# Optimization experiments

Hardware: AMD Instinct MI355X
Metric: run time of the kernel (lower is better)

## Reference

```python
import jax, jax.numpy as jnp
import numpy as np

N = 100000   # nodes
E = 1600000  # edges
IN_DIM = 256
HID = 128
OUT_DIM = 64
LAYERS = 3
LN_EPS = 1e-5


def _layer_norm(y, g, b):
    mu = jnp.mean(y, axis=-1, keepdims=True)
    var = jnp.mean(jnp.square(y - mu), axis=-1, keepdims=True)
    return (y - mu) * jax.lax.rsqrt(var + LN_EPS) * g + b


def _gcn_conv(x, W, b, src, dst, norm):
    # x: [N, H]; W: [H, H]; src/dst: [E+N] (self-loops appended); norm: [E+N]
    xw = x @ W
    msg = xw[src] * norm[:, None]                       # [E+N, H] gather
    out = jax.ops.segment_sum(msg, dst, num_segments=N)  # scatter-add
    return out + b


def setup_inputs() -> dict:
    key = jax.random.key(0)
    ks = jax.random.split(key, 8)
    x = jax.random.normal(ks[0], (N, IN_DIM), dtype=jnp.float32)
    edge_index = jax.random.randint(ks[1], (2, E), 0, N, dtype=jnp.int32)
    in_W = jax.random.normal(ks[2], (IN_DIM, HID), dtype=jnp.float32) / np.sqrt(IN_DIM).astype(np.float32)
    in_b = jnp.zeros((HID,), jnp.float32)
    conv_W = jax.random.normal(ks[3], (LAYERS, HID, HID), dtype=jnp.float32) / np.sqrt(HID).astype(np.float32)
    conv_b = jnp.zeros((LAYERS, HID), jnp.float32)
    ln_g = jnp.ones((LAYERS, HID), jnp.float32)
    ln_b = jnp.zeros((LAYERS, HID), jnp.float32)
    out_W = jax.random.normal(ks[4], (HID, OUT_DIM), dtype=jnp.float32) / np.sqrt(HID).astype(np.float32)
    out_b = jnp.zeros((OUT_DIM,), jnp.float32)
    return {"x": x, "edge_index": edge_index, "in_W": in_W, "in_b": in_b,
            "conv_W": conv_W, "conv_b": conv_b, "ln_g": ln_g, "ln_b": ln_b,
            "out_W": out_W, "out_b": out_b}


def reference(x, edge_index, in_W, in_b, conv_W, conv_b, ln_g, ln_b, out_W, out_b):
    # add self loops (GCNConv add_self_loops=True, edge_weight=None -> ones)
    loops = jnp.arange(N, dtype=edge_index.dtype)
    src = jnp.concatenate([edge_index[0], loops])
    dst = jnp.concatenate([edge_index[1], loops])
    # symmetric normalization: deg over destination, norm = d^-1/2[src]*d^-1/2[dst]
    deg = jax.ops.segment_sum(jnp.ones_like(src, dtype=jnp.float32), dst, num_segments=N)
    dinv = jnp.where(deg > 0, jax.lax.rsqrt(deg), 0.0)
    norm = dinv[src] * dinv[dst]

    h = x @ in_W + in_b
    for i in range(LAYERS):
        y = _gcn_conv(h, conv_W[i], conv_b[i], src, dst, norm)
        y = _layer_norm(y, ln_g[i], ln_b[i])
        y = jax.nn.relu(y)
        h = h + y  # residual (dropout is identity in eval mode)
    return h @ out_W + out_b
```

## Files before the change

### kernel.cpp

```cpp
#include <hip/hip_runtime.h>
#include <hip/hip_bf16.h>

#define N_NODES 100000
#define E_EDGES 1600000
#define IN_DIM  256
#define HID     128
#define OUT_DIM 64
#define LAYERS  3
#define LN_EPS  1e-5f

typedef __attribute__((ext_vector_type(8)))  short bf16x8;
typedef __attribute__((ext_vector_type(16))) float f32x16;

__device__ inline short f2bf(float f) {
    unsigned u = __float_as_uint(f);
    unsigned r = (u + 0x7fffu + ((u >> 16) & 1u)) >> 16;
    return (short)r;
}
__device__ inline float bflo(unsigned u) { return __uint_as_float(u << 16); }
__device__ inline float bfhi(unsigned u) { return __uint_as_float(u & 0xffff0000u); }


__global__ __launch_bounds__(256) void deg_kernel(const int* __restrict__ dst, int* __restrict__ deg) {
    int e = blockIdx.x * 256 + threadIdx.x;
    if (e < E_EDGES) atomicAdd(&deg[dst[e]], 1);
}

__global__ __launch_bounds__(256) void dinv_kernel(const int* __restrict__ deg, float* __restrict__ dinv) {
    int i = blockIdx.x * 256 + threadIdx.x;
    if (i < N_NODES) dinv[i] = rsqrtf((float)(deg[i] + 1));
}


#define NB_SCAN ((N_NODES + 255) / 256)

__global__ __launch_bounds__(256) void block_sum_kernel(const int* __restrict__ deg,
                                                        int* __restrict__ blockSums) {
    __shared__ int s[256];
    int i = blockIdx.x * 256 + threadIdx.x;
    s[threadIdx.x] = (i < N_NODES) ? deg[i] : 0;
    __syncthreads();
#pragma unroll
    for (int o = 128; o; o >>= 1) {
        if (threadIdx.x < o) s[threadIdx.x] += s[threadIdx.x + o];
        __syncthreads();
    }
    if (threadIdx.x == 0) blockSums[blockIdx.x] = s[0];
}

__global__ __launch_bounds__(512) void scan_blocks_kernel(int* __restrict__ blockSums, int nb) {
    __shared__ int s[512];
    int t = threadIdx.x;
    int orig = (t < nb) ? blockSums[t] : 0;
    s[t] = orig;
    __syncthreads();
#pragma unroll
    for (int o = 1; o < 512; o <<= 1) {
        int v = (t >= o) ? s[t - o] : 0;
        __syncthreads();
        s[t] += v;
        __syncthreads();
    }
    if (t < nb) blockSums[t] = s[t] - orig;
}

__global__ __launch_bounds__(256) void scan_final_kernel(const int* __restrict__ deg,
                                                         const int* __restrict__ blockSums,
                                                         int* __restrict__ offsets,
                                                         int* __restrict__ cursor) {
    __shared__ int s[256];
    int i = blockIdx.x * 256 + threadIdx.x;
    int t = threadIdx.x;
    int v = (i < N_NODES) ? deg[i] : 0;
    s[t] = v;
    __syncthreads();
#pragma unroll
    for (int o = 1; o < 256; o <<= 1) {
        int u = (t >= o) ? s[t - o] : 0;
        __syncthreads();
        s[t] += u;
        __syncthreads();
    }
    if (i < N_NODES) {
        int excl = s[t] - v + blockSums[blockIdx.x];
        offsets[i] = excl;
        cursor[i] = excl;
    }
}

__global__ __launch_bounds__(256) void bin_kernel(const int* __restrict__ src,
                                                  const int* __restrict__ dst,
                                                  const float* __restrict__ dinv,
                                                  int* __restrict__ cursor,
                                                  int2* __restrict__ es) {
    int e = blockIdx.x * 256 + threadIdx.x;
    if (e >= E_EDGES) return;
    int s = src[e], d = dst[e];
    int p = atomicAdd(&cursor[d], 1);
    es[p] = make_int2(s, __float_as_int(dinv[s] * dinv[d]));
}


template<int K, int N>
__global__ __launch_bounds__(256) void wt_kernel(const float* __restrict__ W, short* __restrict__ WT) {
    int idx = blockIdx.x * 256 + threadIdx.x;
    if (idx >= K * N) return;
    int n = idx / K, k = idx % K;
    WT[idx] = f2bf(W[(long)k * N + n]);
}


template<int KT, int N, bool ABF>
__global__ __launch_bounds__(256) void mfma_gemm(const void* __restrict__ Av,
                                                 const short* __restrict__ WT,
                                                 const float* __restrict__ bias,
                                                 float* __restrict__ C,
                                                 short* __restrict__ Cb,
                                                 int M) {
    constexpr int BK = 128;
    constexpr int SR = BK * 2 + 16;
    constexpr int NT = N / 32;

    __shared__ char lds[N * SR];

    const int tid = threadIdx.x;
    const int wv = tid >> 6;
    const int ln = tid & 63;
    const int l31 = ln & 31;
    const int lh = ln >> 5;
    const int row_base = blockIdx.x * 256 + wv * 64;

    f32x16 acc[2][NT];
#pragma unroll
    for (int rt = 0; rt < 2; rt++)
#pragma unroll
        for (int nt = 0; nt < NT; nt++)
#pragma unroll
            for (int r = 0; r < 16; r++) acc[rt][nt][r] = 0.f;

    long aoff[2];
#pragma unroll
    for (int rt = 0; rt < 2; rt++) {
        int r = row_base + rt * 32 + l31;
        if (r > M - 1) r = M - 1;
        aoff[rt] = (long)r * KT + lh * 8;
    }

#pragma unroll
    for (int c = 0; c < KT / BK; c++) {
        __syncthreads();
#pragma unroll
        for (int i = tid; i < N * 16; i += 256) {
            int n = i >> 4, kb = (i & 15) << 4;
            float4 v = *(const float4*)((const char*)WT + (long)n * (KT * 2) + c * (BK * 2) + kb);
            *(float4*)(&lds[n * SR + kb]) = v;
        }
        __syncthreads();

#pragma unroll
        for (int ks = 0; ks < BK / 16; ks++) {
            bf16x8 a[2];
#pragma unroll
            for (int rt = 0; rt < 2; rt++) {
                if (ABF) {
                    a[rt] = *(const bf16x8*)((const short*)Av + aoff[rt] + c * BK + ks * 16);
                } else {
                    const float* ap = (const float*)Av + aoff[rt] + c * BK + ks * 16;
                    float4 f0 = *(const float4*)(ap);
                    float4 f1 = *(const float4*)(ap + 4);
                    bf16x8 t;
                    t[0] = f2bf(f0.x); t[1] = f2bf(f0.y); t[2] = f2bf(f0.z); t[3] = f2bf(f0.w);
                    t[4] = f2bf(f1.x); t[5] = f2bf(f1.y); t[6] = f2bf(f1.z); t[7] = f2bf(f1.w);
                    a[rt] = t;
                }
            }
            bf16x8 b[NT];
#pragma unroll
            for (int nt = 0; nt < NT; nt++) {
                int n = nt * 32 + l31;
                b[nt] = *(const bf16x8*)(&lds[n * SR + ks * 32 + lh * 16]);
            }
#pragma unroll
            for (int nt = 0; nt < NT; nt++) {
                acc[0][nt] = __builtin_amdgcn_mfma_f32_32x32x16_bf16(a[0], b[nt], acc[0][nt], 0, 0, 0);
                acc[1][nt] = __builtin_amdgcn_mfma_f32_32x32x16_bf16(a[1], b[nt], acc[1][nt], 0, 0, 0);
            }
        }
    }

#pragma unroll
    for (int rt = 0; rt < 2; rt++) {
#pragma unroll
        for (int nt = 0; nt < NT; nt++) {
            int col = nt * 32 + l31;
            float bv = bias ? bias[col] : 0.f;
#pragma unroll
            for (int r = 0; r < 16; r++) {
                int row = row_base + rt * 32 + (r & 3) + 8 * (r >> 2) + 4 * lh;
                if (row < M) {
                    float v = acc[rt][nt][r] + bv;
                    if (C)  C[(long)row * N + col] = v;
                    if (Cb) Cb[(long)row * N + col] = f2bf(v);
                }
            }
        }
    }
}


__global__ __launch_bounds__(256) void gather_post_kernel(const int* __restrict__ offsets,
                                                          const int* __restrict__ deg,
                                                          const int2* __restrict__ es,
                                                          const float* __restrict__ dinv,
                                                          const short* __restrict__ xwb,
                                                          const float* __restrict__ b,
                                                          const float* __restrict__ g,
                                                          const float* __restrict__ beta,
                                                          float* __restrict__ h,
                                                          short* __restrict__ hb) {
    int wave = threadIdx.x >> 6;
    int lane = threadIdx.x & 63;
    int row = blockIdx.x * 4 + wave;
    if (row >= N_NODES) return;

    const int2* ep = es + offsets[row];
    int dg = deg[row];

    float acc0 = 0.f, acc1 = 0.f;
    int j = 0;
    for (; j + 4 <= dg; j += 4) {
        int2 e0 = ep[j + 0];
        int2 e1 = ep[j + 1];
        int2 e2 = ep[j + 2];
        int2 e3 = ep[j + 3];
        unsigned u0 = *(const unsigned*)(&xwb[(long)e0.x * HID + lane * 2]);
        unsigned u1 = *(const unsigned*)(&xwb[(long)e1.x * HID + lane * 2]);
        unsigned u2 = *(const unsigned*)(&xwb[(long)e2.x * HID + lane * 2]);
        unsigned u3 = *(const unsigned*)(&xwb[(long)e3.x * HID + lane * 2]);
        float w0 = __int_as_float(e0.y), w1 = __int_as_float(e1.y);
        float w2 = __int_as_float(e2.y), w3 = __int_as_float(e3.y);
        acc0 += bflo(u0) * w0; acc1 += bfhi(u0) * w0;
        acc0 += bflo(u1) * w1; acc1 += bfhi(u1) * w1;
        acc0 += bflo(u2) * w2; acc1 += bfhi(u2) * w2;
        acc0 += bflo(u3) * w3; acc1 += bfhi(u3) * w3;
    }
    for (; j < dg; j++) {
        int2 e0 = ep[j];
        float w0 = __int_as_float(e0.y);
        unsigned u0 = *(const unsigned*)(&xwb[(long)e0.x * HID + lane * 2]);
        acc0 += bflo(u0) * w0; acc1 += bfhi(u0) * w0;
    }

    float di = dinv[row];
    float sw = di * di;
    unsigned ux = *(const unsigned*)(&xwb[(long)row * HID + lane * 2]);
    float2 bv = *reinterpret_cast<const float2*>(&b[lane * 2]);
    float y0 = acc0 + bflo(ux) * sw + bv.x;
    float y1 = acc1 + bfhi(ux) * sw + bv.y;

    float sum = y0 + y1;
#pragma unroll
    for (int o = 32; o; o >>= 1) sum += __shfl_xor(sum, o);
    float mu = sum * (1.0f / HID);

    float d0 = y0 - mu, d1 = y1 - mu;
    float vs = d0 * d0 + d1 * d1;
#pragma unroll
    for (int o = 32; o; o >>= 1) vs += __shfl_xor(vs, o);
    float rstd = rsqrtf(vs * (1.0f / HID) + LN_EPS);

    float2 gv = *reinterpret_cast<const float2*>(&g[lane * 2]);
    float2 bev = *reinterpret_cast<const float2*>(&beta[lane * 2]);
    float r0 = fmaxf(d0 * rstd * gv.x + bev.x, 0.0f);
    float r1 = fmaxf(d1 * rstd * gv.y + bev.y, 0.0f);

    float2* hp = reinterpret_cast<float2*>(&h[(long)row * HID + lane * 2]);
    float2 hv = *hp;
    hv.x += r0;
    hv.y += r1;
    *hp = hv;

    unsigned pk = ((unsigned)(unsigned short)f2bf(hv.y) << 16) |
                  (unsigned)(unsigned short)f2bf(hv.x);
    *reinterpret_cast<unsigned*>(&hb[(long)row * HID + lane * 2]) = pk;
}


extern "C" void kernel_launch(void* const* d_in, const int* in_sizes, int n_in,
                              void* d_out, int out_size, void* d_ws, size_t ws_size,
                              hipStream_t stream) {
    const float* x      = (const float*)d_in[0];
    const int*   eidx   = (const int*)d_in[1];
    const float* in_W   = (const float*)d_in[2];
    const float* in_b   = (const float*)d_in[3];
    const float* conv_W = (const float*)d_in[4];
    const float* conv_b = (const float*)d_in[5];
    const float* ln_g   = (const float*)d_in[6];
    const float* ln_b   = (const float*)d_in[7];
    const float* out_W  = (const float*)d_in[8];
    const float* out_b  = (const float*)d_in[9];

    const int* src = eidx;
    const int* dst = eidx + E_EDGES;

    char* ws = (char*)d_ws;
    size_t off = 0;
    auto alloc = [&](size_t bytes) {
        void* p = ws + off;
        off += (bytes + 1023) & ~(size_t)1023;
        return p;
    };
    int*   deg       = (int*)  alloc((size_t)N_NODES * 4);
    float* dinv      = (float*)alloc((size_t)N_NODES * 4);
    int*   offsets   = (int*)  alloc((size_t)N_NODES * 4);
    int*   cursor    = (int*)  alloc((size_t)N_NODES * 4);
    int*   blockSums = (int*)  alloc((size_t)NB_SCAN * 4);
    int2*  es        = (int2*) alloc((size_t)E_EDGES * 8);
    float* h         = (float*)alloc((size_t)N_NODES * HID * 4);
    short* hb        = (short*)alloc((size_t)N_NODES * HID * 2);
    short* xwb       = (short*)alloc((size_t)N_NODES * HID * 2);
    short* in_WT     = (short*)alloc((size_t)IN_DIM * HID * 2);
    short* conv_WT   = (short*)alloc((size_t)LAYERS * HID * HID * 2);
    short* out_WT    = (short*)alloc((size_t)HID * OUT_DIM * 2);

    hipMemsetAsync(deg, 0, (size_t)N_NODES * 4, stream);
    deg_kernel<<<(E_EDGES + 255) / 256, 256, 0, stream>>>(dst, deg);
    dinv_kernel<<<(N_NODES + 255) / 256, 256, 0, stream>>>(deg, dinv);

    block_sum_kernel<<<NB_SCAN, 256, 0, stream>>>(deg, blockSums);
    scan_blocks_kernel<<<1, 512, 0, stream>>>(blockSums, NB_SCAN);
    scan_final_kernel<<<NB_SCAN, 256, 0, stream>>>(deg, blockSums, offsets, cursor);
    bin_kernel<<<(E_EDGES + 255) / 256, 256, 0, stream>>>(src, dst, dinv, cursor, es);

    wt_kernel<IN_DIM, HID><<<(IN_DIM * HID + 255) / 256, 256, 0, stream>>>(in_W, in_WT);
    for (int l = 0; l < LAYERS; l++)
        wt_kernel<HID, HID><<<(HID * HID + 255) / 256, 256, 0, stream>>>(
            conv_W + (size_t)l * HID * HID, conv_WT + (size_t)l * HID * HID);
    wt_kernel<HID, OUT_DIM><<<(HID * OUT_DIM + 255) / 256, 256, 0, stream>>>(out_W, out_WT);

    const int ggrid = (N_NODES + 255) / 256;

    mfma_gemm<IN_DIM, HID, false><<<ggrid, 256, 0, stream>>>(
        (const void*)x, in_WT, in_b, h, hb, N_NODES);

    for (int l = 0; l < LAYERS; l++) {
        mfma_gemm<HID, HID, true><<<ggrid, 256, 0, stream>>>(
            (const void*)hb, conv_WT + (size_t)l * HID * HID, nullptr, nullptr, xwb, N_NODES);
        gather_post_kernel<<<(N_NODES + 3) / 4, 256, 0, stream>>>(
            offsets, deg, es, dinv, xwb,
            conv_b + l * HID, ln_g + l * HID, ln_b + l * HID, h, hb);
    }

    mfma_gemm<HID, OUT_DIM, true><<<ggrid, 256, 0, stream>>>(
        (const void*)hb, out_WT, out_b, (float*)d_out, nullptr, N_NODES);
}
```

Before: 800.2 us.

## Drop LDS staging of weights in MFMA GEMM; load B fragments directly from global

The GEMM kernel no longer copies the transposed weight tile into shared memory behind barriers. Each wave now loads its B fragments straight from global memory (relying on L1/L2 caching of the small weight matrix) and computes 32 rows instead of 64. Block row count is halved and the grid doubled. This removes the LDS copy and syncthreads cost and lowers register pressure, but each wave re-reads the weights from cache and gets half the A reuse per B load.

Result: faster. 783.5 us (-2.1%).

```diff
diff --git a/kernel.cpp b/kernel.cpp
--- a/kernel.cpp
+++ b/kernel.cpp
@@ -117,91 +117,63 @@
                                                  float* __restrict__ C,
                                                  short* __restrict__ Cb,
                                                  int M) {
-    constexpr int BK = 128;
-    constexpr int SR = BK * 2 + 16;
     constexpr int NT = N / 32;
-
-    __shared__ char lds[N * SR];
 
     const int tid = threadIdx.x;
     const int wv = tid >> 6;
     const int ln = tid & 63;
     const int l31 = ln & 31;
     const int lh = ln >> 5;
-    const int row_base = blockIdx.x * 256 + wv * 64;
-
-    f32x16 acc[2][NT];
-#pragma unroll
-    for (int rt = 0; rt < 2; rt++)
+    const int row0 = blockIdx.x * 128 + wv * 32;
+
+    int ar = row0 + l31;
+    if (ar > M - 1) ar = M - 1;
+
+    const short* abf = (const short*)Av + (long)ar * KT + lh * 8;
+    const float* af32 = (const float*)Av + (long)ar * KT + lh * 8;
+    const short* bbase[NT];
+#pragma unroll
+    for (int nt = 0; nt < NT; nt++)
+        bbase[nt] = WT + (long)(nt * 32 + l31) * KT + lh * 8;
+
+    f32x16 acc[NT];
+#pragma unroll
+    for (int nt = 0; nt < NT; nt++)
+#pragma unroll
+        for (int r = 0; r < 16; r++) acc[nt][r] = 0.f;
+
+#pragma unroll
+    for (int ks = 0; ks < KT / 16; ks++) {
+        bf16x8 a;
+        if (ABF) {
+            a = *(const bf16x8*)(abf + ks * 16);
+        } else {
+            float4 f0 = *(const float4*)(af32 + ks * 16);
+            float4 f1 = *(const float4*)(af32 + ks * 16 + 4);
+            bf16x8 t;
+            t[0] = f2bf(f0.x); t[1] = f2bf(f0.y); t[2] = f2bf(f0.z); t[3] = f2bf(f0.w);
+            t[4] = f2bf(f1.x); t[5] = f2bf(f1.y); t[6] = f2bf(f1.z); t[7] = f2bf(f1.w);
+            a = t;
+        }
+        bf16x8 b[NT];
+#pragma unroll
+        for (int nt = 0; nt < NT; nt++) b[nt] = *(const bf16x8*)(bbase[nt] + ks * 16);
 #pragma unroll
         for (int nt = 0; nt < NT; nt++)
-#pragma unroll
-            for (int r = 0; r < 16; r++) acc[rt][nt][r] = 0.f;
-
-    long aoff[2];
-#pragma unroll
-    for (int rt = 0; rt < 2; rt++) {
-        int r = row_base + rt * 32 + l31;
-        if (r > M - 1) r = M - 1;
-        aoff[rt] = (long)r * KT + lh * 8;
-    }
-
-#pragma unroll
-    for (int c = 0; c < KT / BK; c++) {
-        __syncthreads();
-#pragma unroll
-        for (int i = tid; i < N * 16; i += 256) {
-            int n = i >> 4, kb = (i & 15) << 4;
-            float4 v = *(const float4*)((const char*)WT + (long)n * (KT * 2) + c * (BK * 2) + kb);
-            *(float4*)(&lds[n * SR + kb]) = v;
-        }
-        __syncthreads();
-
-#pragma unroll
-        for (int ks = 0; ks < BK / 16; ks++) {
-            bf16x8 a[2];
-#pragma unroll
-            for (int rt = 0; rt < 2; rt++) {
-                if (ABF) {
-                    a[rt] = *(const bf16x8*)((const short*)Av + aoff[rt] + c * BK + ks * 16);
-                } else {
-                    const float* ap = (const float*)Av + aoff[rt] + c * BK + ks * 16;
-                    float4 f0 = *(const float4*)(ap);
-                    float4 f1 = *(const float4*)(ap + 4);
-                    bf16x8 t;
-                    t[0] = f2bf(f0.x); t[1] = f2bf(f0.y); t[2] = f2bf(f0.z); t[3] = f2bf(f0.w);
-                    t[4] = f2bf(f1.x); t[5] = f2bf(f1.y); t[6] = f2bf(f1.z); t[7] = f2bf(f1.w);
-                    a[rt] = t;
-                }
-            }
-            bf16x8 b[NT];
-#pragma unroll
-            for (int nt = 0; nt < NT; nt++) {
-                int n = nt * 32 + l31;
-                b[nt] = *(const bf16x8*)(&lds[n * SR + ks * 32 + lh * 16]);
-            }
-#pragma unroll
-            for (int nt = 0; nt < NT; nt++) {
-                acc[0][nt] = __builtin_amdgcn_mfma_f32_32x32x16_bf16(a[0], b[nt], acc[0][nt], 0, 0, 0);
-                acc[1][nt] = __builtin_amdgcn_mfma_f32_32x32x16_bf16(a[1], b[nt], acc[1][nt], 0, 0, 0);
-            }
-        }
-    }
-
-#pragma unroll
-    for (int rt = 0; rt < 2; rt++) {
-#pragma unroll
-        for (int nt = 0; nt < NT; nt++) {
-            int col = nt * 32 + l31;
-            float bv = bias ? bias[col] : 0.f;
-#pragma unroll
-            for (int r = 0; r < 16; r++) {
-                int row = row_base + rt * 32 + (r & 3) + 8 * (r >> 2) + 4 * lh;
-                if (row < M) {
-                    float v = acc[rt][nt][r] + bv;
-                    if (C)  C[(long)row * N + col] = v;
-                    if (Cb) Cb[(long)row * N + col] = f2bf(v);
-                }
+            acc[nt] = __builtin_amdgcn_mfma_f32_32x32x16_bf16(a, b[nt], acc[nt], 0, 0, 0);
+    }
+
+#pragma unroll
+    for (int nt = 0; nt < NT; nt++) {
+        int col = nt * 32 + l31;
+        float bv = bias ? bias[col] : 0.f;
+#pragma unroll
+        for (int r = 0; r < 16; r++) {
+            int row = row0 + (r & 3) + 8 * (r >> 2) + 4 * lh;
+            if (row < M) {
+                float v = acc[nt][r] + bv;
+                if (C)  C[(long)row * N + col] = v;
+                if (Cb) Cb[(long)row * N + col] = f2bf(v);
             }
         }
     }
@@ -338,7 +310,7 @@
             conv_W + (size_t)l * HID * HID, conv_WT + (size_t)l * HID * HID);
     wt_kernel<HID, OUT_DIM><<<(HID * OUT_DIM + 255) / 256, 256, 0, stream>>>(out_W, out_WT);
 
-    const int ggrid = (N_NODES + 255) / 256;
+    const int ggrid = (N_NODES + 127) / 128;
 
     mfma_gemm<IN_DIM, HID, false><<<ggrid, 256, 0, stream>>>(
         (const void*)x, in_WT, in_b, h, hb, N_NODES);
```
